# Performance work log

Hardware: AMD Instinct MI355X
Metric: run time of the kernel (lower is better)

## Reference

```python
import jax, jax.numpy as jnp
import numpy as np

N = 50000   # nodes
E = 800000  # edges
B = 50      # graphs
EPS = 1e-5


def setup_inputs() -> dict:
    key = jax.random.key(0)
    ks = jax.random.split(key, 32)
    x = jax.random.normal(ks[0], (N, 128), dtype=jnp.float32)
    edge_index = jax.random.randint(ks[1], (2, E), 0, N, dtype=jnp.int32)
    batch = jnp.sort(jax.random.randint(ks[2], (N,), 0, B, dtype=jnp.int32))
    dims = [(128, 256), (256, 512), (512, 256), (256, 128)]
    inp = {"x": x, "edge_index": edge_index, "batch": batch}
    ki = 3
    for i, (cin, cout) in enumerate(dims, start=1):
        s = 1.0 / np.sqrt(cin)
        inp[f"conv{i}_W"] = jax.random.uniform(ks[ki], (3, cin, cout), jnp.float32, -s, s); ki += 1
        inp[f"conv{i}_b"] = jax.random.uniform(ks[ki], (cout,), jnp.float32, -s, s); ki += 1
        inp[f"gn{i}_w"] = jnp.ones((cout,), jnp.float32)
        inp[f"gn{i}_b"] = jnp.zeros((cout,), jnp.float32)
        inp[f"gn{i}_ms"] = jnp.ones((cout,), jnp.float32)
    inp["lin1_W"] = jax.random.uniform(ks[ki], (128, 64), jnp.float32, -1/np.sqrt(128), 1/np.sqrt(128)); ki += 1
    inp["lin1_b"] = jnp.zeros((64,), jnp.float32)
    inp["lin2_W"] = jax.random.uniform(ks[ki], (64, 10), jnp.float32, -1/np.sqrt(64), 1/np.sqrt(64)); ki += 1
    inp["lin2_b"] = jnp.zeros((10,), jnp.float32)
    return inp


def _cheb_conv(x, src, dst, nw, W, b):
    # PyG ChebConv, K=3, sym norm, lambda_max=2 => L_hat = -D^-1/2 A D^-1/2
    def prop(h):
        return jax.ops.segment_sum(nw[:, None] * h[src], dst, num_segments=N)
    Tx0 = x
    Tx1 = prop(x)
    Tx2 = 2.0 * prop(Tx1) - Tx0
    return Tx0 @ W[0] + Tx1 @ W[1] + Tx2 @ W[2] + b


def _graph_norm(x, batch, cnt, w, b, ms):
    mean = jax.ops.segment_sum(x, batch, num_segments=B) / cnt[:, None]
    sub = x - ms * mean[batch]
    var = jax.ops.segment_sum(sub * sub, batch, num_segments=B) / cnt[:, None]
    return w * sub * jax.lax.rsqrt(var[batch] + EPS) + b


def reference(x, edge_index, batch,
              conv1_W, conv1_b, gn1_w, gn1_b, gn1_ms,
              conv2_W, conv2_b, gn2_w, gn2_b, gn2_ms,
              conv3_W, conv3_b, gn3_w, gn3_b, gn3_ms,
              conv4_W, conv4_b, gn4_w, gn4_b, gn4_ms,
              lin1_W, lin1_b, lin2_W, lin2_b):
    src, dst = edge_index[0], edge_index[1]
    deg = jax.ops.segment_sum(jnp.ones((E,), x.dtype), dst, num_segments=N)
    dinv = jnp.where(deg > 0, jax.lax.rsqrt(jnp.maximum(deg, 1.0)), 0.0)
    nw = -dinv[src] * dinv[dst]  # scaled-Laplacian edge weights
    cnt = jnp.maximum(jax.ops.segment_sum(jnp.ones((N,), x.dtype), batch, num_segments=B), 1.0)

    h = x
    layers = [(conv1_W, conv1_b, gn1_w, gn1_b, gn1_ms),
              (conv2_W, conv2_b, gn2_w, gn2_b, gn2_ms),
              (conv3_W, conv3_b, gn3_w, gn3_b, gn3_ms),
              (conv4_W, conv4_b, gn4_w, gn4_b, gn4_ms)]
    for (W, bb, gw, gb, gms) in layers:
        h = _cheb_conv(h, src, dst, nw, W, bb)
        h = _graph_norm(h, batch, cnt, gw, gb, gms)
        h = jnp.where(h >= 0, h, 0.2 * h)  # leaky_relu(0.2)
    h = h + x  # residual
    pooled = jax.ops.segment_sum(h, batch, num_segments=B) / cnt[:, None]
    out = jnp.tanh(pooled @ lin1_W + lin1_b)
    return out @ lin2_W + lin2_b
```

## Files before the change

### kernel.cpp

```cpp
#include <hip/hip_runtime.h>

#define NN 50000
#define EE 800000
#define BG 50

typedef unsigned short ushort_t;
typedef __bf16 bf16x8 __attribute__((ext_vector_type(8)));
typedef float f32x4 __attribute__((ext_vector_type(4)));

__device__ __forceinline__ float b2f(ushort_t h) {
    unsigned int u = ((unsigned int)h) << 16;
    float f; __builtin_memcpy(&f, &u, 4); return f;
}
__device__ __forceinline__ ushort_t f2b(float f) {
    unsigned int u; __builtin_memcpy(&u, &f, 4);
    unsigned int r = u + 0x7fffu + ((u >> 16) & 1u);
    return (ushort_t)(r >> 16);
}

__device__ __forceinline__ void async_ld16(const void* g, void* l) {
    __builtin_amdgcn_global_load_lds(
        (__attribute__((address_space(1))) unsigned int*)(void*)g,
        (__attribute__((address_space(3))) unsigned int*)l, 16, 0, 0);
}

__global__ void k_detect(const ushort_t* xs, int* flag) {
    __shared__ int cnt;
    if (threadIdx.x == 0) cnt = 0;
    __syncthreads();
    int e = (xs[2 * threadIdx.x] >> 7) & 0xFF;
    if (e >= 96 && e <= 142) atomicAdd(&cnt, 1);
    __syncthreads();
    if (threadIdx.x == 0) *flag = (cnt >= 300) ? 1 : 0;
}

struct CastJobs {
    const void* src[25];
    int off[25];
    int start[26];
};
__global__ void k_castall(CastJobs jb, ushort_t* base, const int* flag, int total) {
    int i = blockIdx.x * 256 + threadIdx.x;
    if (i >= total) return;
    int lo = 0;
    while (i >= jb.start[lo + 1]) ++lo;
    int k = i - jb.start[lo];
    const void* s = jb.src[lo];
    ushort_t v;
    if (*flag) v = ((const ushort_t*)s)[k];
    else       v = f2b(((const float*)s)[k]);
    base[jb.off[lo] + k] = v;
}

__global__ void k_deg(const int* edge, int* degi) {
    int e = blockIdx.x * 256 + threadIdx.x;
    if (e < EE) atomicAdd(&degi[edge[EE + e]], 1);
}
__global__ void k_gcnt(const int* batch, float* cntf) {
    int g = threadIdx.x;
    if (g >= BG) return;
    int lo = 0, hi = NN;
    while (lo < hi) { int m = (lo + hi) >> 1; if (batch[m] < g) lo = m + 1; else hi = m; }
    int a = lo; lo = 0; hi = NN;
    while (lo < hi) { int m = (lo + hi) >> 1; if (batch[m] < g + 1) lo = m + 1; else hi = m; }
    cntf[g] = fmaxf((float)(lo - a), 1.0f);
}
__global__ void k_scan1(const int* degi, int* rowptr, int* bsum, float* dinv) {
    __shared__ int sh[1024];
    int t = threadIdx.x, i = blockIdx.x * 1024 + t;
    int v = (i < NN) ? degi[i] : 0;
    if (i < NN) dinv[i] = v > 0 ? rsqrtf((float)v) : 0.0f;
    sh[t] = v; __syncthreads();
    for (int off = 1; off < 1024; off <<= 1) {
        int add = (t >= off) ? sh[t - off] : 0;
        __syncthreads();
        sh[t] += add;
        __syncthreads();
    }
    if (i < NN) rowptr[i] = sh[t] - v;
    if (t == 1023) bsum[blockIdx.x] = sh[t];
}
__global__ void k_scan2(const int* bsum, int* boff, int* rowptr) {
    if (threadIdx.x == 0) {
        int run = 0;
        for (int j = 0; j < 49; ++j) { boff[j] = run; run += bsum[j]; }
        rowptr[NN] = run;
    }
}
__global__ void k_scan3(int* rowptr, const int* boff) {
    int i = blockIdx.x * 256 + threadIdx.x;
    if (i < NN) rowptr[i] += boff[i >> 10];
}
__global__ void k_fill(const int* edge, const float* dinv, const int* rowptr,
                       int* cursor, int* csrc, float* cw) {
    int e = blockIdx.x * 256 + threadIdx.x;
    if (e >= EE) return;
    int s = edge[e], d = edge[EE + e];
    int slot = atomicAdd(&cursor[d], 1);
    int pos = rowptr[d] + slot;
    csrc[pos] = s;
    cw[pos] = -dinv[s] * dinv[d];
}

__global__ void k_transpose(const ushort_t* W, ushort_t* WT, int K, int C) {
    __shared__ ushort_t tile[32][33];
    int bx = blockIdx.x * 32, by = blockIdx.y * 32;
    int tx = threadIdx.x, ty = threadIdx.y;
    for (int i = ty; i < 32; i += 8) tile[i][tx] = W[(size_t)(bx + i) * C + by + tx];
    __syncthreads();
    for (int i = ty; i < 32; i += 8) WT[(size_t)(by + i) * K + bx + tx] = tile[tx][i];
}

template<int SL>
__launch_bounds__(256)
__global__ void k_prop3(ushort_t* out, int ldo,
                        const ushort_t* src, int lds_, int soff,
                        const ushort_t* addP, int lda_, int aoff,
                        const ushort_t* subP, int ldsu, int suoff,
                        const ushort_t* bias, float alpha,
                        const int* rowptr, const int* csrc, const float* cw) {
    constexpr int EG = 64 / SL;
    int n = blockIdx.x * 4 + (threadIdx.x >> 6);
    if (n >= NN) return;
    int lane = threadIdx.x & 63;
    int eg = lane / SL;
    int cpos = (lane % SL) * 8;
    int r0 = rowptr[n], r1 = rowptr[n + 1];
    float acc[8];
#pragma unroll
    for (int i = 0; i < 8; ++i) acc[i] = 0.f;
    const ushort_t* sbase = src + soff + cpos;
    int j = r0 + eg;
    for (; j + EG < r1; j += 2 * EG) {
        int s0 = csrc[j], s1 = csrc[j + EG];
        float w0 = cw[j], w1 = cw[j + EG];
        __bf16 v0[8], v1[8];
        __builtin_memcpy(v0, sbase + (size_t)s0 * lds_, 16);
        __builtin_memcpy(v1, sbase + (size_t)s1 * lds_, 16);
#pragma unroll
        for (int i = 0; i < 8; ++i) acc[i] += w0 * (float)v0[i];
#pragma unroll
        for (int i = 0; i < 8; ++i) acc[i] += w1 * (float)v1[i];
    }
    if (j < r1) {
        int s0 = csrc[j]; float w0 = cw[j];
        __bf16 v0[8];
        __builtin_memcpy(v0, sbase + (size_t)s0 * lds_, 16);
#pragma unroll
        for (int i = 0; i < 8; ++i) acc[i] += w0 * (float)v0[i];
    }
#pragma unroll
    for (int off = SL; off < 64; off <<= 1)
#pragma unroll
        for (int i = 0; i < 8; ++i) acc[i] += __shfl_xor(acc[i], off);

    if (eg == 0) {
        float res[8];
#pragma unroll
        for (int i = 0; i < 8; ++i) res[i] = alpha * acc[i];
        if (addP) {
            __bf16 a[8];
            __builtin_memcpy(a, addP + (size_t)n * lda_ + aoff + cpos, 16);
#pragma unroll
            for (int i = 0; i < 8; ++i) res[i] += (float)a[i];
        }
        if (subP) {
            __bf16 sm[8];
            __builtin_memcpy(sm, subP + (size_t)n * ldsu + suoff + cpos, 16);
#pragma unroll
            for (int i = 0; i < 8; ++i) res[i] -= (float)sm[i];
        }
        if (bias) {
            __bf16 bb[8];
            __builtin_memcpy(bb, bias + cpos, 16);
#pragma unroll
            for (int i = 0; i < 8; ++i) res[i] += (float)bb[i];
        }
        ushort_t o[8];
#pragma unroll
        for (int i = 0; i < 8; ++i) o[i] = f2b(res[i]);
        __builtin_memcpy(out + (size_t)n * ldo + cpos, o, 16);
    }
}

__launch_bounds__(256)
__global__ void k_gemm(const ushort_t* A0, const ushort_t* A1, const ushort_t* A2,
                       int lda, const ushort_t* WT, const ushort_t* bias, int hasBias,
                       ushort_t* out, int ldout, int Ktot) {
    __shared__ __align__(16) ushort_t ldsA[128 * 64];
    __shared__ __align__(16) ushort_t ldsB[128 * 64];
    const int tid = threadIdx.x, lane = tid & 63, w = tid >> 6;
    const int wm = w & 1, wn = w >> 1;
    const int m0 = blockIdx.x * 128, n0 = blockIdx.y * 128;
    const int KT = Ktot / 64, per = lda >> 6;

    f32x4 acc[4][4];
#pragma unroll
    for (int i = 0; i < 4; ++i)
#pragma unroll
        for (int j = 0; j < 4; ++j) acc[i][j] = (f32x4){0.f, 0.f, 0.f, 0.f};

    const int srow = lane >> 3;
    const int scolX = (((lane & 7) ^ srow) << 3);
    const int l7 = lane & 7;

    for (int kt = 0; kt < KT; ++kt) {
        int seg = kt / per, lk = (kt - seg * per) * 64;
        const ushort_t* Ap = (seg == 0) ? A0 : ((seg == 1) ? A1 : A2);
        __syncthreads();
#pragma unroll
        for (int t = 0; t < 4; ++t) {
            int inst = (w << 2) + t;
            int row = inst * 8 + srow;
            int gr = m0 + row; if (gr >= NN) gr = NN - 1;
            async_ld16(Ap + (size_t)gr * lda + lk + scolX, &ldsA[inst * 512]);
            async_ld16(WT + (size_t)(n0 + row) * Ktot + kt * 64 + scolX, &ldsB[inst * 512]);
        }
        __builtin_amdgcn_s_waitcnt(0);
        __syncthreads();
#pragma unroll
        for (int kk = 0; kk < 64; kk += 32) {
            bf16x8 aF[4], bF[4];
            int qx = ((((kk >> 3) + (lane >> 4)) ^ l7) << 3);
#pragma unroll
            for (int i = 0; i < 4; ++i) {
                aF[i] = *(const bf16x8*)&ldsA[(wm * 64 + i * 16 + (lane & 15)) * 64 + qx];
                bF[i] = *(const bf16x8*)&ldsB[(wn * 64 + i * 16 + (lane & 15)) * 64 + qx];
            }
#pragma unroll
            for (int i = 0; i < 4; ++i)
#pragma unroll
                for (int j = 0; j < 4; ++j)
                    acc[i][j] = __builtin_amdgcn_mfma_f32_16x16x32_bf16(aF[i], bF[j], acc[i][j], 0, 0, 0);
        }
    }
#pragma unroll
    for (int i = 0; i < 4; ++i) {
        int rbase = m0 + wm * 64 + i * 16 + ((lane >> 4) << 2);
#pragma unroll
        for (int j = 0; j < 4; ++j) {
            int col = n0 + wn * 64 + j * 16 + (lane & 15);
            float bv = hasBias ? b2f(bias[col]) : 0.0f;
#pragma unroll
            for (int r = 0; r < 4; ++r) {
                int row = rbase + r;
                if (row < NN) out[(size_t)row * ldout + col] = f2b(acc[i][j][r] + bv);
            }
        }
    }
}

__global__ void k_stats(const ushort_t* h, const int* batch, float* sums, float* sumsq,
                        int C, int withSq) {
    int c = blockIdx.y * 128 + threadIdx.x;
    int na = blockIdx.x * 128, nb = na + 128 < NN ? na + 128 : NN;
    int cur = -1; float s = 0.f, sq = 0.f;
    for (int n = na; n < nb; ++n) {
        int g = batch[n];
        if (g != cur) {
            if (cur >= 0) { atomicAdd(&sums[cur * C + c], s); if (withSq) atomicAdd(&sumsq[cur * C + c], sq); }
            cur = g; s = 0.f; sq = 0.f;
        }
        float v = b2f(h[(size_t)n * C + c]);
        s += v; sq += v * v;
    }
    if (cur >= 0) { atomicAdd(&sums[cur * C + c], s); if (withSq) atomicAdd(&sumsq[cur * C + c], sq); }
}

template<int VEC>
__launch_bounds__(256)
__global__ void k_norm2(const ushort_t* hpre, const int* batch, const float* sums,
                        const float* sumsq, const float* cntf,
                        const ushort_t* gw, const ushort_t* gb, const ushort_t* gms,
                        const ushort_t* xres, ushort_t* out, int addres) {
    constexpr int C = VEC * 64;
    int n = blockIdx.x * 4 + (threadIdx.x >> 6);
    if (n >= NN) return;
    int lane = threadIdx.x & 63;
    int coff = lane * VEC;
    int g = batch[n];
    float cg = cntf[g];
    float sm[VEC], sq[VEC];
    __builtin_memcpy(sm, sums  + g * C + coff, VEC * 4);
    __builtin_memcpy(sq, sumsq + g * C + coff, VEC * 4);
    __bf16 vgw[VEC], vgb[VEC], vms[VEC], vh[VEC];
    __builtin_memcpy(vgw, gw + coff, VEC * 2);
    __builtin_memcpy(vgb, gb + coff, VEC * 2);
    __builtin_memcpy(vms, gms + coff, VEC * 2);
    __builtin_memcpy(vh, hpre + (size_t)n * C + coff, VEC * 2);
    __bf16 vx[VEC];
    if (addres) __builtin_memcpy(vx, xres + (size_t)n * 128 + coff, VEC * 2);
    ushort_t o[VEC];
#pragma unroll
    for (int i = 0; i < VEC; ++i) {
        float mean = sm[i] / cg;
        float ms = (float)vms[i];
        float var = sq[i] / cg - mean * mean * ms * (2.0f - ms);
        var = fmaxf(var, 0.0f);
        float y = (float)vgw[i] * ((float)vh[i] - ms * mean) * rsqrtf(var + 1e-5f) + (float)vgb[i];
        y = (y >= 0.0f) ? y : 0.2f * y;
        if (addres) y += (float)vx[i];
        o[i] = f2b(y);
    }
    __builtin_memcpy(out + (size_t)n * C + coff, o, VEC * 2);
}

__global__ void k_head(const float* pooled, const float* cntf,
                       const ushort_t* W1, const ushort_t* b1,
                       const ushort_t* W2, const ushort_t* b2s, void* out,
                       const int* flag) {
    __shared__ float pl[128];
    __shared__ float hid[64];
    int g = blockIdx.x, t = threadIdx.x;
    float inv = 1.0f / cntf[g];
    for (int k = t; k < 128; k += 64) pl[k] = pooled[g * 128 + k] * inv;
    __syncthreads();
    float a = b2f(b1[t]);
    for (int k = 0; k < 128; ++k) a += pl[k] * b2f(W1[k * 64 + t]);
    hid[t] = tanhf(a);
    __syncthreads();
    if (t < 10) {
        float o = b2f(b2s[t]);
        for (int j = 0; j < 64; ++j) o += hid[j] * b2f(W2[j * 10 + t]);
        if (*flag) ((ushort_t*)out)[g * 10 + t] = f2b(o);
        else       ((float*)out)[g * 10 + t]    = o;
    }
}

extern "C" void kernel_launch(void* const* d_in, const int* in_sizes, int n_in,
                              void* d_out, int out_size, void* d_ws, size_t ws_size,
                              hipStream_t stream) {
    (void)in_sizes; (void)n_in; (void)out_size; (void)ws_size;

    const void* x_raw = d_in[0];
    const int* edge   = (const int*)d_in[1];
    const int* batch  = (const int*)d_in[2];

    char* ws = (char*)d_ws;
    float*    dinv   = (float*)   (ws + 0);
    int*      degi   = (int*)     (ws + 200192);
    int*      rowptr = (int*)     (ws + 400384);
    int*      cursor = (int*)     (ws + 600576);
    int*      bsum   = (int*)     (ws + 800768);
    int*      boff   = (int*)     (ws + 801024);
    float*    cntf   = (float*)   (ws + 801280);
    float*    sums   = (float*)   (ws + 801536);
    float*    sumsq  = (float*)   (ws + 903936);
    float*    pooled = (float*)   (ws + 1006336);
    int*      dflag  = (int*)     (ws + 1031936);
    ushort_t* Xb     = (ushort_t*)(ws + 1032192);
    ushort_t* Wst    = (ushort_t*)(ws + 13832192);
    ushort_t* WTall  = (ushort_t*)(ws + 15798272);
    ushort_t* SB     = (ushort_t*)(ws + 17764352);
    int*      csrc   = (int*)     (ws + 17791488);
    float*    cw     = (float*)   (ws + 20991488);
    ushort_t* T1     = (ushort_t*)(ws + 24191488);
    ushort_t* T2     = (ushort_t*)(ws + 75391488);
    ushort_t* P      = (ushort_t*)(ws + 126591488);
    ushort_t* HA     = (ushort_t*)(ws + 177791488);

    const int cins[4]  = {128, 256, 512, 256};
    const int couts[4] = {256, 512, 256, 128};
    const size_t wtoff[4] = {0, 98304, 491520, 884736};
    const int bo[4] = {0, 256, 768, 1024};
    const int gwo = 1152, gbo = 2304, gmo = 3456;
    const int l1Wo = 4608, l1bo = 12800, l2Wo = 12864, l2bo = 13504;

    const int XB_E = 1032192 / 2, WST_E = 13832192 / 2, SB_E = 17764352 / 2;

    CastJobs jb;
    int sizes[25]; int nj = 0;
    auto addjob = [&](const void* s, int off, int n) {
        jb.src[nj] = s; jb.off[nj] = off; sizes[nj] = n; ++nj;
    };
    addjob(x_raw, XB_E, NN * 128);
    for (int l = 0; l < 4; ++l) {
        addjob(d_in[3 + 5 * l], WST_E + (int)wtoff[l], 3 * cins[l] * couts[l]);
        addjob(d_in[4 + 5 * l], SB_E + bo[l],        couts[l]);
        addjob(d_in[5 + 5 * l], SB_E + gwo + bo[l],  couts[l]);
        addjob(d_in[6 + 5 * l], SB_E + gbo + bo[l],  couts[l]);
        addjob(d_in[7 + 5 * l], SB_E + gmo + bo[l],  couts[l]);
    }
    addjob(d_in[23], SB_E + l1Wo, 128 * 64);
    addjob(d_in[24], SB_E + l1bo, 64);
    addjob(d_in[25], SB_E + l2Wo, 64 * 10);
    addjob(d_in[26], SB_E + l2bo, 10);
    int run = 0;
    for (int k = 0; k < 25; ++k) { jb.start[k] = run; run += sizes[k]; }
    jb.start[25] = run;

    k_detect<<<1, 512, 0, stream>>>((const ushort_t*)x_raw, dflag);
    hipMemsetAsync(degi,   0, NN * 4, stream);
    hipMemsetAsync(cursor, 0, NN * 4, stream);
    hipMemsetAsync(pooled, 0, BG * 128 * 4, stream);

    k_castall<<<(run + 255) / 256, 256, 0, stream>>>(jb, (ushort_t*)ws, dflag, run);

    k_deg<<<(EE + 255) / 256, 256, 0, stream>>>(edge, degi);
    k_gcnt<<<1, 64, 0, stream>>>(batch, cntf);
    k_scan1<<<49, 1024, 0, stream>>>(degi, rowptr, bsum, dinv);
    k_scan2<<<1, 64, 0, stream>>>(bsum, boff, rowptr);
    k_scan3<<<(NN + 255) / 256, 256, 0, stream>>>(rowptr, boff);
    k_fill<<<(EE + 255) / 256, 256, 0, stream>>>(edge, dinv, rowptr, cursor, csrc, cw);

    for (int l = 0; l < 2; ++l) {
        dim3 g((3 * cins[l]) / 32, couts[l] / 32);
        k_transpose<<<g, dim3(32, 8), 0, stream>>>(Wst + wtoff[l], WTall + wtoff[l],
                                                   3 * cins[l], couts[l]);
    }
    for (int l = 2; l < 4; ++l) {
        dim3 g(cins[l] / 32, couts[l] / 32);
        for (int j = 0; j < 3; ++j)
            k_transpose<<<g, dim3(32, 8), 0, stream>>>(
                Wst + wtoff[l] + (size_t)j * cins[l] * couts[l],
                WTall + wtoff[l] + (size_t)j * couts[l] * cins[l],
                cins[l], couts[l]);
    }

    const int NB = (NN + 3) / 4;
    auto prop = [&](int C, ushort_t* o, int ldo,
                    const ushort_t* s, int lds_, int soff,
                    const ushort_t* aP, int lda_, int aoff,
                    const ushort_t* sP, int ldsu, int suoff,
                    const ushort_t* bias, float alpha) {
        if (C == 128)
            k_prop3<16><<<NB, 256, 0, stream>>>(o, ldo, s, lds_, soff, aP, lda_, aoff,
                                                sP, ldsu, suoff, bias, alpha, rowptr, csrc, cw);
        else
            k_prop3<32><<<NB, 256, 0, stream>>>(o, ldo, s, lds_, soff, aP, lda_, aoff,
                                                sP, ldsu, suoff, bias, alpha, rowptr, csrc, cw);
    };
    auto norm = [&](int C, const ushort_t* hp, const ushort_t* gwp, const ushort_t* gbp,
                    const ushort_t* gmp, ushort_t* o, int addres) {
        if (C == 128)      k_norm2<2><<<NB, 256, 0, stream>>>(hp, batch, sums, sumsq, cntf, gwp, gbp, gmp, Xb, o, addres);
        else if (C == 256) k_norm2<4><<<NB, 256, 0, stream>>>(hp, batch, sums, sumsq, cntf, gwp, gbp, gmp, Xb, o, addres);
        else               k_norm2<8><<<NB, 256, 0, stream>>>(hp, batch, sums, sumsq, cntf, gwp, gbp, gmp, Xb, o, addres);
    };

    ushort_t* G = T1;
    const ushort_t* hin = Xb;
    for (int l = 0; l < 4; ++l) {
        int cin = cins[l], cout = couts[l];
        if (l < 2) {
            prop(cin, T1, cin, hin, cin, 0, nullptr, 0, 0, nullptr, 0, 0, nullptr, 1.0f);
            prop(cin, T2, cin, T1, cin, 0, nullptr, 0, 0, hin, cin, 0, nullptr, 2.0f);
            k_gemm<<<dim3((NN + 127) / 128, cout / 128), 256, 0, stream>>>(
                hin, T1, T2, cin, WTall + wtoff[l], SB + bo[l], 1, P, cout, 3 * cin);
        } else {
            k_gemm<<<dim3((NN + 127) / 128, (3 * cout) / 128), 256, 0, stream>>>(
                hin, hin, hin, cin, WTall + wtoff[l], nullptr, 0, G, 3 * cout, cin);
            ushort_t* V = HA;
            prop(cout, V, cout, G, 3 * cout, 2 * cout, G, 3 * cout, cout,
                 nullptr, 0, 0, nullptr, 2.0f);
            prop(cout, P, cout, V, cout, 0, G, 3 * cout, 0,
                 G, 3 * cout, 2 * cout, SB + bo[l], 1.0f);
        }
        hipMemsetAsync(sums, 0, 2 * 102400, stream);
        k_stats<<<dim3((NN + 127) / 128, cout / 128), 128, 0, stream>>>(P, batch, sums, sumsq, cout, 1);
        norm(cout, P, SB + gwo + bo[l], SB + gbo + bo[l], SB + gmo + bo[l], HA, l == 3);
        hin = HA;
    }
    k_stats<<<dim3((NN + 127) / 128, 1), 128, 0, stream>>>(HA, batch, pooled, pooled, 128, 0);
    k_head<<<BG, 64, 0, stream>>>(pooled, cntf, SB + l1Wo, SB + l1bo, SB + l2Wo, SB + l2bo,
                                  d_out, dflag);
}
```

Baseline: 1.212 ms.

## Pack CSR edges, unroll gather by four, swap GEMM grid order, vectorize stats

```diff
diff --git a/kernel.cpp b/kernel.cpp
--- a/kernel.cpp
+++ b/kernel.cpp
@@ -92,14 +92,15 @@
     if (i < NN) rowptr[i] += boff[i >> 10];
 }
 __global__ void k_fill(const int* edge, const float* dinv, const int* rowptr,
-                       int* cursor, int* csrc, float* cw) {
+                       int* cursor, int2* epack) {
     int e = blockIdx.x * 256 + threadIdx.x;
     if (e >= EE) return;
     int s = edge[e], d = edge[EE + e];
     int slot = atomicAdd(&cursor[d], 1);
     int pos = rowptr[d] + slot;
-    csrc[pos] = s;
-    cw[pos] = -dinv[s] * dinv[d];
+    float wv = -dinv[s] * dinv[d];
+    int2 pk; pk.x = s; __builtin_memcpy(&pk.y, &wv, 4);
+    epack[pos] = pk;
 }
 
 __global__ void k_transpose(const ushort_t* W, ushort_t* WT, int K, int C) {
@@ -118,7 +119,7 @@
                         const ushort_t* addP, int lda_, int aoff,
                         const ushort_t* subP, int ldsu, int suoff,
                         const ushort_t* bias, float alpha,
-                        const int* rowptr, const int* csrc, const float* cw) {
+                        const int* rowptr, const int2* epack) {
     constexpr int EG = 64 / SL;
     int n = blockIdx.x * 4 + (threadIdx.x >> 6);
     if (n >= NN) return;
@@ -131,23 +132,28 @@
     for (int i = 0; i < 8; ++i) acc[i] = 0.f;
     const ushort_t* sbase = src + soff + cpos;
     int j = r0 + eg;
-    for (; j + EG < r1; j += 2 * EG) {
-        int s0 = csrc[j], s1 = csrc[j + EG];
-        float w0 = cw[j], w1 = cw[j + EG];
-        __bf16 v0[8], v1[8];
-        __builtin_memcpy(v0, sbase + (size_t)s0 * lds_, 16);
-        __builtin_memcpy(v1, sbase + (size_t)s1 * lds_, 16);
-#pragma unroll
-        for (int i = 0; i < 8; ++i) acc[i] += w0 * (float)v0[i];
-#pragma unroll
-        for (int i = 0; i < 8; ++i) acc[i] += w1 * (float)v1[i];
-    }
-    if (j < r1) {
-        int s0 = csrc[j]; float w0 = cw[j];
+    for (; j + 3 * EG < r1; j += 4 * EG) {
+        int2 p[4];
+#pragma unroll
+        for (int u = 0; u < 4; ++u) p[u] = epack[j + u * EG];
+        __bf16 v[4][8];
+#pragma unroll
+        for (int u = 0; u < 4; ++u)
+            __builtin_memcpy(v[u], sbase + (size_t)p[u].x * lds_, 16);
+#pragma unroll
+        for (int u = 0; u < 4; ++u) {
+            float wv; __builtin_memcpy(&wv, &p[u].y, 4);
+#pragma unroll
+            for (int i = 0; i < 8; ++i) acc[i] += wv * (float)v[u][i];
+        }
+    }
+    for (; j < r1; j += EG) {
+        int2 p0 = epack[j];
+        float wv; __builtin_memcpy(&wv, &p0.y, 4);
         __bf16 v0[8];
-        __builtin_memcpy(v0, sbase + (size_t)s0 * lds_, 16);
-#pragma unroll
-        for (int i = 0; i < 8; ++i) acc[i] += w0 * (float)v0[i];
+        __builtin_memcpy(v0, sbase + (size_t)p0.x * lds_, 16);
+#pragma unroll
+        for (int i = 0; i < 8; ++i) acc[i] += wv * (float)v0[i];
     }
 #pragma unroll
     for (int off = SL; off < 64; off <<= 1)
@@ -191,7 +197,7 @@
     __shared__ __align__(16) ushort_t ldsB[128 * 64];
     const int tid = threadIdx.x, lane = tid & 63, w = tid >> 6;
     const int wm = w & 1, wn = w >> 1;
-    const int m0 = blockIdx.x * 128, n0 = blockIdx.y * 128;
+    const int m0 = blockIdx.y * 128, n0 = blockIdx.x * 128;
     const int KT = Ktot / 64, per = lda >> 6;
 
     f32x4 acc[4][4];
@@ -250,21 +256,44 @@
     }
 }
 
-__global__ void k_stats(const ushort_t* h, const int* batch, float* sums, float* sumsq,
-                        int C, int withSq) {
-    int c = blockIdx.y * 128 + threadIdx.x;
-    int na = blockIdx.x * 128, nb = na + 128 < NN ? na + 128 : NN;
-    int cur = -1; float s = 0.f, sq = 0.f;
-    for (int n = na; n < nb; ++n) {
+template<int VEC>
+__launch_bounds__(256)
+__global__ void k_stats2(const ushort_t* h, const int* batch, float* sums, float* sumsq,
+                         int withSq) {
+    constexpr int C = VEC * 64;
+    int wave = threadIdx.x >> 6, lane = threadIdx.x & 63;
+    int n0 = blockIdx.x * 128 + wave * 32;
+    if (n0 >= NN) return;
+    int n1 = n0 + 32 < NN ? n0 + 32 : NN;
+    int coff = lane * VEC;
+    float s[VEC], sq[VEC];
+#pragma unroll
+    for (int i = 0; i < VEC; ++i) { s[i] = 0.f; sq[i] = 0.f; }
+    int cur = batch[n0];
+    for (int n = n0; n < n1; ++n) {
         int g = batch[n];
         if (g != cur) {
-            if (cur >= 0) { atomicAdd(&sums[cur * C + c], s); if (withSq) atomicAdd(&sumsq[cur * C + c], sq); }
-            cur = g; s = 0.f; sq = 0.f;
-        }
-        float v = b2f(h[(size_t)n * C + c]);
-        s += v; sq += v * v;
-    }
-    if (cur >= 0) { atomicAdd(&sums[cur * C + c], s); if (withSq) atomicAdd(&sumsq[cur * C + c], sq); }
+#pragma unroll
+            for (int i = 0; i < VEC; ++i) {
+                atomicAdd(&sums[cur * C + coff + i], s[i]);
+                if (withSq) atomicAdd(&sumsq[cur * C + coff + i], sq[i]);
+                s[i] = 0.f; sq[i] = 0.f;
+            }
+            cur = g;
+        }
+        __bf16 v[VEC];
+        __builtin_memcpy(v, h + (size_t)n * C + coff, VEC * 2);
+#pragma unroll
+        for (int i = 0; i < VEC; ++i) {
+            float f = (float)v[i];
+            s[i] += f; sq[i] += f * f;
+        }
+    }
+#pragma unroll
+    for (int i = 0; i < VEC; ++i) {
+        atomicAdd(&sums[cur * C + coff + i], s[i]);
+        if (withSq) atomicAdd(&sumsq[cur * C + coff + i], sq[i]);
+    }
 }
 
 template<int VEC>
@@ -352,8 +381,7 @@
     ushort_t* Wst    = (ushort_t*)(ws + 13832192);
     ushort_t* WTall  = (ushort_t*)(ws + 15798272);
     ushort_t* SB     = (ushort_t*)(ws + 17764352);
-    int*      csrc   = (int*)     (ws + 17791488);
-    float*    cw     = (float*)   (ws + 20991488);
+    int2*     epack  = (int2*)    (ws + 17791488);
     ushort_t* T1     = (ushort_t*)(ws + 24191488);
     ushort_t* T2     = (ushort_t*)(ws + 75391488);
     ushort_t* P      = (ushort_t*)(ws + 126591488);
@@ -401,7 +429,7 @@
     k_scan1<<<49, 1024, 0, stream>>>(degi, rowptr, bsum, dinv);
     k_scan2<<<1, 64, 0, stream>>>(bsum, boff, rowptr);
     k_scan3<<<(NN + 255) / 256, 256, 0, stream>>>(rowptr, boff);
-    k_fill<<<(EE + 255) / 256, 256, 0, stream>>>(edge, dinv, rowptr, cursor, csrc, cw);
+    k_fill<<<(EE + 255) / 256, 256, 0, stream>>>(edge, dinv, rowptr, cursor, epack);
 
     for (int l = 0; l < 2; ++l) {
         dim3 g((3 * cins[l]) / 32, couts[l] / 32);
@@ -418,6 +446,7 @@
     }
 
     const int NB = (NN + 3) / 4;
+    const int SBk = (NN + 127) / 128;
     auto prop = [&](int C, ushort_t* o, int ldo,
                     const ushort_t* s, int lds_, int soff,
                     const ushort_t* aP, int lda_, int aoff,
@@ -425,10 +454,15 @@
                     const ushort_t* bias, float alpha) {
         if (C == 128)
             k_prop3<16><<<NB, 256, 0, stream>>>(o, ldo, s, lds_, soff, aP, lda_, aoff,
-                                                sP, ldsu, suoff, bias, alpha, rowptr, csrc, cw);
+                                                sP, ldsu, suoff, bias, alpha, rowptr, epack);
         else
             k_prop3<32><<<NB, 256, 0, stream>>>(o, ldo, s, lds_, soff, aP, lda_, aoff,
-                                                sP, ldsu, suoff, bias, alpha, rowptr, csrc, cw);
+                                                sP, ldsu, suoff, bias, alpha, rowptr, epack);
+    };
+    auto stats = [&](int C, const ushort_t* h, float* sm, float* sq, int withSq) {
+        if (C == 128)      k_stats2<2><<<SBk, 256, 0, stream>>>(h, batch, sm, sq, withSq);
+        else if (C == 256) k_stats2<4><<<SBk, 256, 0, stream>>>(h, batch, sm, sq, withSq);
+        else               k_stats2<8><<<SBk, 256, 0, stream>>>(h, batch, sm, sq, withSq);
     };
     auto norm = [&](int C, const ushort_t* hp, const ushort_t* gwp, const ushort_t* gbp,
                     const ushort_t* gmp, ushort_t* o, int addres) {
@@ -444,10 +478,10 @@
         if (l < 2) {
             prop(cin, T1, cin, hin, cin, 0, nullptr, 0, 0, nullptr, 0, 0, nullptr, 1.0f);
             prop(cin, T2, cin, T1, cin, 0, nullptr, 0, 0, hin, cin, 0, nullptr, 2.0f);
-            k_gemm<<<dim3((NN + 127) / 128, cout / 128), 256, 0, stream>>>(
+            k_gemm<<<dim3(cout / 128, (NN + 127) / 128), 256, 0, stream>>>(
                 hin, T1, T2, cin, WTall + wtoff[l], SB + bo[l], 1, P, cout, 3 * cin);
         } else {
-            k_gemm<<<dim3((NN + 127) / 128, (3 * cout) / 128), 256, 0, stream>>>(
+            k_gemm<<<dim3((3 * cout) / 128, (NN + 127) / 128), 256, 0, stream>>>(
                 hin, hin, hin, cin, WTall + wtoff[l], nullptr, 0, G, 3 * cout, cin);
             ushort_t* V = HA;
             prop(cout, V, cout, G, 3 * cout, 2 * cout, G, 3 * cout, cout,
@@ -456,11 +490,11 @@
                  G, 3 * cout, 2 * cout, SB + bo[l], 1.0f);
         }
         hipMemsetAsync(sums, 0, 2 * 102400, stream);
-        k_stats<<<dim3((NN + 127) / 128, cout / 128), 128, 0, stream>>>(P, batch, sums, sumsq, cout, 1);
+        stats(cout, P, sums, sumsq, 1);
         norm(cout, P, SB + gwo + bo[l], SB + gbo + bo[l], SB + gmo + bo[l], HA, l == 3);
         hin = HA;
     }
-    k_stats<<<dim3((NN + 127) / 128, 1), 128, 0, stream>>>(HA, batch, pooled, pooled, 128, 0);
+    stats(128, HA, pooled, pooled, 0);
     k_head<<<BG, 64, 0, stream>>>(pooled, cntf, SB + l1Wo, SB + l1bo, SB + l2Wo, SB + l2bo,
                                   d_out, dflag);
 }
```

Result: faster. 1.104 ms (-8.9%).
